# Performance work log

Measured on AMD Instinct MI355X. Metric: run time of the kernel, lower is better.

Reference implementation:

```python
import jax, jax.numpy as jnp
import numpy as np

EMBED_DIM = 2048
NUM_HEADS = 32
NUM_KV_HEADS = 8
HEAD_DIM = EMBED_DIM // NUM_HEADS          # 64
GROUP = NUM_HEADS // NUM_KV_HEADS          # 4 queries per KV head
BATCH, SEQ = 2, 2048


def setup_inputs() -> dict:
    key = jax.random.key(0)
    ks = jax.random.split(key, 9)
    s_in = 1.0 / np.sqrt(EMBED_DIM)
    kv_dim = NUM_KV_HEADS * HEAD_DIM
    return {
        "x":      jax.random.normal(ks[0], (BATCH, SEQ, EMBED_DIM), jnp.float32),
        "Wq":     jax.random.normal(ks[1], (EMBED_DIM, EMBED_DIM), jnp.float32) * s_in,
        "bq":     jnp.zeros((EMBED_DIM,), jnp.float32),
        "Wk":     jax.random.normal(ks[2], (EMBED_DIM, kv_dim), jnp.float32) * s_in,
        "bk":     jnp.zeros((kv_dim,), jnp.float32),
        "Wv":     jax.random.normal(ks[3], (EMBED_DIM, kv_dim), jnp.float32) * s_in,
        "bv":     jnp.zeros((kv_dim,), jnp.float32),
        "Wo":     jax.random.normal(ks[4], (EMBED_DIM, EMBED_DIM), jnp.float32) * s_in,
        "bo":     jnp.zeros((EMBED_DIM,), jnp.float32),
    }


def reference(x, Wq, bq, Wk, bk, Wv, bv, Wo, bo):
    B, S, _ = x.shape
    # Projections (torch Linear == x @ W + b with W stored as [in, out] here)
    q = (x @ Wq + bq).reshape(B, S, NUM_KV_HEADS, GROUP, HEAD_DIM)  # grouped heads
    k = (x @ Wk + bk).reshape(B, S, NUM_KV_HEADS, HEAD_DIM)
    v = (x @ Wv + bv).reshape(B, S, NUM_KV_HEADS, HEAD_DIM)

    scale = 1.0 / np.sqrt(HEAD_DIM)
    # scores[b, h, g, s, t] = q[b, s, h, g, :] . k[b, t, h, :]
    # (repeat_interleave of K across the group dim == broadcasting over g)
    scores = jnp.einsum("bshgd,bthd->bhgst", q, k) * scale
    attn = jax.nn.softmax(scores, axis=-1)
    out = jnp.einsum("bhgst,bthd->bshgd", attn, v)  # [B, S, kvh, g, D]
    out = out.reshape(B, S, EMBED_DIM)
    return out @ Wo + bo
```

## Files before the change

### kernel.cpp

```cpp
#include <hip/hip_runtime.h>


typedef __attribute__((ext_vector_type(8)))  short     s16x8;
typedef __attribute__((ext_vector_type(8)))  _Float16  h8;
typedef __attribute__((ext_vector_type(2)))  __fp16    fp16x2;
typedef __attribute__((ext_vector_type(4)))  float     f32x4;
typedef __attribute__((ext_vector_type(16))) float     f32x16;

#define DEVI static __device__ __forceinline__

#if __has_builtin(__builtin_amdgcn_exp2f)
#define EXP2F __builtin_amdgcn_exp2f
#else
#define EXP2F exp2f
#endif

DEVI short f2h(float f){ _Float16 h = (_Float16)f; return __builtin_bit_cast(short, h); }
DEVI unsigned pkh(float a, float b){
  fp16x2 t = __builtin_amdgcn_cvt_pkrtz(a, b);
  return __builtin_bit_cast(unsigned, t);
}

typedef __attribute__((address_space(3))) unsigned       lds_u32;
typedef __attribute__((address_space(1))) const unsigned gbl_u32;
DEVI void glds16(const short* g, short* l){
  __builtin_amdgcn_global_load_lds((gbl_u32*)g, (lds_u32*)l, 16, 0, 0);
}

__global__ void cast_kernel(const float* __restrict__ in, short* __restrict__ out, int n){
  int i = (blockIdx.x * 256 + threadIdx.x) * 8;
  if(i >= n) return;
  float4 a = *(const float4*)(in + i);
  float4 b = *(const float4*)(in + i + 4);
  s16x8 v;
  v[0]=f2h(a.x); v[1]=f2h(a.y); v[2]=f2h(a.z); v[3]=f2h(a.w);
  v[4]=f2h(b.x); v[5]=f2h(b.y); v[6]=f2h(b.z); v[7]=f2h(b.w);
  *(s16x8*)(out + i) = v;
}

__global__ void prep_kernel(const float* __restrict__ Wq, const float* __restrict__ Wk,
                            const float* __restrict__ Wv, const float* __restrict__ Wo,
                            const float* __restrict__ bq, const float* __restrict__ bk,
                            const float* __restrict__ bv,
                            short* __restrict__ WT, short* __restrict__ WoT,
                            float* __restrict__ bqkv){
  __shared__ __align__(16) short tile[64*72];
  const int gy = blockIdx.y;
  const int t = threadIdx.x;
  if(gy >= 80){
    int i = blockIdx.x * 256 + t;
    if(i < 3072) bqkv[i] = (i < 2048) ? bq[i] : (i < 2560 ? bk[i-2048] : bv[i-2560]);
    return;
  }
  const float* src; short* dst; int ldin, by;
  if(gy < 32)      { src = Wq; dst = WT;             ldin = 2048; by = gy;    }
  else if(gy < 40) { src = Wk; dst = WT + 2048*2048; ldin =  512; by = gy-32; }
  else if(gy < 48) { src = Wv; dst = WT + 2560*2048; ldin =  512; by = gy-40; }
  else             { src = Wo; dst = WoT;            ldin = 2048; by = gy-48; }
  const int tr = blockIdx.x * 64;
  const int tc = by * 64;
  for(int c = t; c < 512; c += 256){
    int r = c >> 3, g = c & 7;
    const float* p = src + (size_t)(tr + r) * ldin + tc + g*8;
    s16x8 v;
    #pragma unroll
    for(int e = 0; e < 8; e++) v[e] = f2h(p[e]);
    *(s16x8*)&tile[r*72 + g*8] = v;
  }
  __syncthreads();
  for(int c = t; c < 512; c += 256){
    int r = c >> 3, g = c & 7;
    s16x8 v;
    #pragma unroll
    for(int e = 0; e < 8; e++) v[e] = tile[(g*8+e)*72 + r];
    *(s16x8*)(dst + (size_t)(tc + r) * 2048 + tr + g*8) = v;
  }
}

template<bool OUT_F32>
__global__ __launch_bounds__(256, 2)
void gemm_bt_kernel(const short* __restrict__ A, const short* __restrict__ BT,
                    const float* __restrict__ bias, void* __restrict__ C,
                    int M, int N, int K, int scale_cols, float qscale){
  __shared__ __align__(16) short As[2][128*32];
  __shared__ __align__(16) short Bs[2][128*32];
  const int m0 = blockIdx.x * 128;
  const int n0 = blockIdx.y * 128;
  const int tid = threadIdx.x;
  const int wave = tid >> 6, lane = tid & 63;
  const int l16 = lane & 15, quad = lane >> 4;
  const int wm = (wave >> 1) * 64, wn = (wave & 1) * 64;

  const short* gA = A  + (size_t)(m0 + wave*32 + (lane>>2))*K + (lane&3)*8;
  const short* gB = BT + (size_t)(n0 + wave*32 + (lane>>2))*K + (lane&3)*8;
  short* lA0 = As[0] + wave*1024;
  short* lA1 = As[1] + wave*1024;
  short* lB0 = Bs[0] + wave*1024;
  short* lB1 = Bs[1] + wave*1024;

  f32x4 acc[4][4];
  #pragma unroll
  for(int i=0;i<4;i++)
    #pragma unroll
    for(int j=0;j<4;j++) acc[i][j] = (f32x4)(0.0f);

  for(int k0 = 0; k0 < K; k0 += 64){
    glds16(gA + k0,                     lA0);
    glds16(gA + 16*(size_t)K + k0,      lA0 + 512);
    glds16(gA + k0 + 32,                lA1);
    glds16(gA + 16*(size_t)K + k0 + 32, lA1 + 512);
    glds16(gB + k0,                     lB0);
    glds16(gB + 16*(size_t)K + k0,      lB0 + 512);
    glds16(gB + k0 + 32,                lB1);
    glds16(gB + 16*(size_t)K + k0 + 32, lB1 + 512);
    __syncthreads();
    h8 af[4], bfr[4];
    #pragma unroll
    for(int i=0;i<4;i++){
      af[i]  = *(const h8*)&As[0][(wm + i*16 + l16)*32 + quad*8];
      bfr[i] = *(const h8*)&Bs[0][(wn + i*16 + l16)*32 + quad*8];
    }
    #pragma unroll
    for(int i=0;i<4;i++)
      #pragma unroll
      for(int j=0;j<4;j++)
        acc[i][j] = __builtin_amdgcn_mfma_f32_16x16x32_f16(af[i], bfr[j], acc[i][j], 0, 0, 0);
    #pragma unroll
    for(int i=0;i<4;i++){
      af[i]  = *(const h8*)&As[1][(wm + i*16 + l16)*32 + quad*8];
      bfr[i] = *(const h8*)&Bs[1][(wn + i*16 + l16)*32 + quad*8];
    }
    #pragma unroll
    for(int i=0;i<4;i++)
      #pragma unroll
      for(int j=0;j<4;j++)
        acc[i][j] = __builtin_amdgcn_mfma_f32_16x16x32_f16(af[i], bfr[j], acc[i][j], 0, 0, 0);
    __syncthreads();
  }

  #pragma unroll
  for(int j=0;j<4;j++){
    int col = n0 + wn + j*16 + l16;
    float bb = bias[col];
    float sc = (col < scale_cols) ? qscale : 1.0f;
    #pragma unroll
    for(int i=0;i<4;i++){
      #pragma unroll
      for(int r=0;r<4;r++){
        size_t row = (size_t)(m0 + wm + i*16 + quad*4 + r);
        float v = (acc[i][j][r] + bb) * sc;
        if(OUT_F32) ((float*)C)[row*(size_t)N + col] = v;
        else        ((short*)C)[row*(size_t)N + col] = f2h(v);
      }
    }
  }
}

__global__ void fragpack_kernel(const short* __restrict__ QKV,
                                short* __restrict__ Kf, short* __restrict__ Vf){
  __shared__ __align__(16) short kt[64*72];
  __shared__ __align__(16) short vt[64*72];
  const int t = blockIdx.x, kvh = blockIdx.y, b = blockIdx.z;
  const int tid = threadIdx.x;
  const size_t rowbase = (size_t)(b*2048 + t*64);
  for(int c = tid; c < 512; c += 256){
    int r = c >> 3, g = c & 7;
    const short* src = QKV + (rowbase + r)*3072 + kvh*64 + g*8;
    *(s16x8*)&kt[r*72 + g*8] = *(const s16x8*)(src + 2048);
    *(s16x8*)&vt[r*72 + g*8] = *(const s16x8*)(src + 2560);
  }
  __syncthreads();
  const size_t obase = ((size_t)(b*8 + kvh)*32 + t) * 4096;
  for(int ch = tid; ch < 512; ch += 256){
    int kb = ch >> 8, l = ch & 63;
    int c = l & 31, h = l >> 5;
    int ks2 = (ch >> 6) & 3;
    *(s16x8*)(Kf + obase + (size_t)ch*8) =
        *(const s16x8*)&kt[(kb*32 + c)*72 + ks2*16 + h*8];
    int ksp = (ch >> 7) & 1, mb = (ch >> 6) & 1;
    int k0 = kb*32 + ksp*16 + h*4;
    int d  = mb*32 + c;
    s16x8 v;
    #pragma unroll
    for(int j = 0; j < 4; j++){
      v[j]   = vt[(k0 + j)*72 + d];
      v[4+j] = vt[(k0 + 8 + j)*72 + d];
    }
    *(s16x8*)(Vf + obase + (size_t)ch*8) = v;
  }
}

__global__ __launch_bounds__(256, 2)
void attn_kernel(const short* __restrict__ Qg, const short* __restrict__ Kf,
                 const short* __restrict__ Vf, short* __restrict__ Og, int ldq){
  const int L = blockIdx.x;
  const int nid = (L & 7)*64 + (L >> 3);
  const int qt  = nid & 31;
  const int grp = nid >> 5;
  const int kvh = grp & 7, b = grp >> 3;
  const int tid = threadIdx.x;
  const int wave = tid >> 6, lane = tid & 63;
  const int c = lane & 31, h = lane >> 5;
  const int head = kvh*4 + wave;
  const int q0 = qt * 64;

  h8 qreg[4][2];
  #pragma unroll
  for(int ks2=0; ks2<4; ks2++)
    #pragma unroll
    for(int qg=0; qg<2; qg++)
      qreg[ks2][qg] = *(const h8*)(Qg + (size_t)(b*2048 + q0 + qg*32 + c)*ldq
                                      + head*64 + ks2*16 + h*8);

  float lsum[2] = {0.0f, 0.0f};
  f32x16 oacc[2][2];
  #pragma unroll
  for(int qg=0; qg<2; qg++)
    #pragma unroll
    for(int mb=0; mb<2; mb++) oacc[qg][mb] = (f32x16)(0.0f);

  const short* kp = Kf + (size_t)grp * 131072 + lane*8;
  const short* vp = Vf + (size_t)grp * 131072 + lane*8;

  h8 kA[4], vA[4], kB[4], vB[4];

  auto loadf = [&](size_t it, h8* K, h8* V){
    const short* kq = kp + it*2048;
    const short* vq = vp + it*2048;
    #pragma unroll
    for(int i=0;i<4;i++){
      K[i] = *(const h8*)(kq + i*512);
      V[i] = *(const h8*)(vq + i*512);
    }
  };

  auto compute = [&](const h8* K, const h8* V){
    f32x16 st[2];
    st[0] = (f32x16)(0.0f); st[1] = (f32x16)(0.0f);
    #pragma unroll
    for(int ks2=0; ks2<4; ks2++){
      st[0] = __builtin_amdgcn_mfma_f32_32x32x16_f16(K[ks2], qreg[ks2][0], st[0], 0, 0, 0);
      st[1] = __builtin_amdgcn_mfma_f32_32x32x16_f16(K[ks2], qreg[ks2][1], st[1], 0, 0, 0);
    }
    union H8U { h8 v; unsigned u[4]; };
    H8U pk[2][2];
    #pragma unroll
    for(int qg=0; qg<2; qg++){
      float sacc = 0.0f;
      #pragma unroll
      for(int j=0; j<4; j++){
        float pa = EXP2F(st[qg][2*j]);
        float pb = EXP2F(st[qg][2*j+1]);
        sacc += pa + pb;
        pk[qg][0].u[j] = pkh(pa, pb);
      }
      #pragma unroll
      for(int j=0; j<4; j++){
        float pa = EXP2F(st[qg][8+2*j]);
        float pb = EXP2F(st[qg][8+2*j+1]);
        sacc += pa + pb;
        pk[qg][1].u[j] = pkh(pa, pb);
      }
      lsum[qg] += sacc;
    }
    #pragma unroll
    for(int ksp=0; ksp<2; ksp++){
      #pragma unroll
      for(int mb=0; mb<2; mb++){
        oacc[0][mb] = __builtin_amdgcn_mfma_f32_32x32x16_f16(V[ksp*2+mb], pk[0][ksp].v, oacc[0][mb], 0, 0, 0);
        oacc[1][mb] = __builtin_amdgcn_mfma_f32_32x32x16_f16(V[ksp*2+mb], pk[1][ksp].v, oacc[1][mb], 0, 0, 0);
      }
    }
  };

  loadf(0, kA, vA);
  #pragma unroll 1
  for(int it = 0; it < 64; it += 2){
    loadf((size_t)(it+1), kB, vB);
    compute(kA, vA);
    loadf((size_t)(it+2 < 64 ? it+2 : 0), kA, vA);
    compute(kB, vB);
  }

  #pragma unroll
  for(int qg=0; qg<2; qg++){
    lsum[qg] += __shfl_xor(lsum[qg], 32);
    float li = 1.0f / lsum[qg];
    size_t rowoff = (size_t)(b*2048 + q0 + qg*32 + c)*2048 + head*64;
    #pragma unroll
    for(int mb=0; mb<2; mb++){
      #pragma unroll
      for(int g2=0; g2<4; g2++){
        int d0 = mb*32 + 8*g2 + 4*h;
        uint2 wv;
        wv.x = pkh(oacc[qg][mb][4*g2+0]*li, oacc[qg][mb][4*g2+1]*li);
        wv.y = pkh(oacc[qg][mb][4*g2+2]*li, oacc[qg][mb][4*g2+3]*li);
        *(uint2*)&Og[rowoff + d0] = wv;
      }
    }
  }
}

extern "C" void kernel_launch(void* const* d_in, const int* in_sizes, int n_in,
                              void* d_out, int out_size, void* d_ws, size_t ws_size,
                              hipStream_t stream){
  const float* x  = (const float*)d_in[0];
  const float* Wq = (const float*)d_in[1];
  const float* bq = (const float*)d_in[2];
  const float* Wk = (const float*)d_in[3];
  const float* bk = (const float*)d_in[4];
  const float* Wv = (const float*)d_in[5];
  const float* bv = (const float*)d_in[6];
  const float* Wo = (const float*)d_in[7];
  const float* bo = (const float*)d_in[8];

  char* ws = (char*)d_ws;
  short* WT   = (short*)(ws);
  short* WoT  = (short*)(ws + 25165824);
  short* xb   = (short*)(ws + 33554432);
  short* QKV  = (short*)(ws + 50331648);
  float* bqkv = (float*)(ws + 79691776);
  short* AO   = xb;
  short* Kf   = (short*)(ws);
  short* Vf   = (short*)(ws + 4194304);

  cast_kernel<<<4096, 256, 0, stream>>>(x, xb, 8388608);
  prep_kernel<<<dim3(32,81), 256, 0, stream>>>(Wq, Wk, Wv, Wo, bq, bk, bv, WT, WoT, bqkv);

  gemm_bt_kernel<false><<<dim3(32,24), 256, 0, stream>>>(xb, WT, bqkv, QKV,
                                                         4096, 3072, 2048,
                                                         2048, 0.1803368801111244f);

  fragpack_kernel<<<dim3(32,8,2), 256, 0, stream>>>(QKV, Kf, Vf);

  attn_kernel<<<512, 256, 0, stream>>>(QKV, Kf, Vf, AO, 3072);

  gemm_bt_kernel<true><<<dim3(32,16), 256, 0, stream>>>(AO, WoT, bo, (float*)d_out,
                                                        4096, 2048, 2048, 0, 1.0f);
}
```

Measured before the change: 299.7 us.

## Double-buffer GEMM LDS tiles to prefetch next K-slice during MFMA compute

The projection GEMM now allocates two LDS stages per operand. It issues the global-to-LDS loads for the next 64-wide K slice before running the MFMAs on the current slice, and drops the barrier that sat between load and compute in each iteration. The goal is to hide global memory latency behind matrix math. In exchange, LDS use per block doubles to 64KB, which could limit how many blocks fit on a CU. Correctness also depends on the end-of-loop barrier waiting for the outstanding async LDS loads.

```diff
diff --git a/kernel.cpp b/kernel.cpp
--- a/kernel.cpp
+++ b/kernel.cpp
@@ -82,8 +82,8 @@
 void gemm_bt_kernel(const short* __restrict__ A, const short* __restrict__ BT,
                     const float* __restrict__ bias, void* __restrict__ C,
                     int M, int N, int K, int scale_cols, float qscale){
-  __shared__ __align__(16) short As[2][128*32];
-  __shared__ __align__(16) short Bs[2][128*32];
+  __shared__ __align__(16) short As[16384];
+  __shared__ __align__(16) short Bs[16384];
   const int m0 = blockIdx.x * 128;
   const int n0 = blockIdx.y * 128;
   const int tid = threadIdx.x;
@@ -93,10 +93,8 @@
 
   const short* gA = A  + (size_t)(m0 + wave*32 + (lane>>2))*K + (lane&3)*8;
   const short* gB = BT + (size_t)(n0 + wave*32 + (lane>>2))*K + (lane&3)*8;
-  short* lA0 = As[0] + wave*1024;
-  short* lA1 = As[1] + wave*1024;
-  short* lB0 = Bs[0] + wave*1024;
-  short* lB1 = Bs[1] + wave*1024;
+  short* lAw = As + wave*1024;
+  short* lBw = Bs + wave*1024;
 
   f32x4 acc[4][4];
   #pragma unroll
@@ -104,21 +102,30 @@
     #pragma unroll
     for(int j=0;j<4;j++) acc[i][j] = (f32x4)(0.0f);
 
+#define STAGE(BUF, K0) do{                                                    \
+    short* a_ = lAw + (BUF)*8192;                                             \
+    short* b_ = lBw + (BUF)*8192;                                             \
+    glds16(gA + (K0),                     a_);                                \
+    glds16(gA + 16*(size_t)K + (K0),      a_ + 512);                          \
+    glds16(gA + (K0) + 32,                a_ + 4096);                         \
+    glds16(gA + 16*(size_t)K + (K0) + 32, a_ + 4096 + 512);                   \
+    glds16(gB + (K0),                     b_);                                \
+    glds16(gB + 16*(size_t)K + (K0),      b_ + 512);                          \
+    glds16(gB + (K0) + 32,                b_ + 4096);                         \
+    glds16(gB + 16*(size_t)K + (K0) + 32, b_ + 4096 + 512);                   \
+  }while(0)
+
+  STAGE(0, 0);
+  __syncthreads();
+  int cur = 0;
   for(int k0 = 0; k0 < K; k0 += 64){
-    glds16(gA + k0,                     lA0);
-    glds16(gA + 16*(size_t)K + k0,      lA0 + 512);
-    glds16(gA + k0 + 32,                lA1);
-    glds16(gA + 16*(size_t)K + k0 + 32, lA1 + 512);
-    glds16(gB + k0,                     lB0);
-    glds16(gB + 16*(size_t)K + k0,      lB0 + 512);
-    glds16(gB + k0 + 32,                lB1);
-    glds16(gB + 16*(size_t)K + k0 + 32, lB1 + 512);
-    __syncthreads();
+    if(k0 + 64 < K) STAGE(cur^1, k0 + 64);
     h8 af[4], bfr[4];
+    const int bb = cur*8192;
     #pragma unroll
     for(int i=0;i<4;i++){
-      af[i]  = *(const h8*)&As[0][(wm + i*16 + l16)*32 + quad*8];
-      bfr[i] = *(const h8*)&Bs[0][(wn + i*16 + l16)*32 + quad*8];
+      af[i]  = *(const h8*)&As[bb + (wm + i*16 + l16)*32 + quad*8];
+      bfr[i] = *(const h8*)&Bs[bb + (wn + i*16 + l16)*32 + quad*8];
     }
     #pragma unroll
     for(int i=0;i<4;i++)
@@ -127,8 +134,8 @@
         acc[i][j] = __builtin_amdgcn_mfma_f32_16x16x32_f16(af[i], bfr[j], acc[i][j], 0, 0, 0);
     #pragma unroll
     for(int i=0;i<4;i++){
-      af[i]  = *(const h8*)&As[1][(wm + i*16 + l16)*32 + quad*8];
-      bfr[i] = *(const h8*)&Bs[1][(wn + i*16 + l16)*32 + quad*8];
+      af[i]  = *(const h8*)&As[bb + 4096 + (wm + i*16 + l16)*32 + quad*8];
+      bfr[i] = *(const h8*)&Bs[bb + 4096 + (wn + i*16 + l16)*32 + quad*8];
     }
     #pragma unroll
     for(int i=0;i<4;i++)
@@ -136,7 +143,9 @@
       for(int j=0;j<4;j++)
         acc[i][j] = __builtin_amdgcn_mfma_f32_16x16x32_f16(af[i], bfr[j], acc[i][j], 0, 0, 0);
     __syncthreads();
-  }
+    cur ^= 1;
+  }
+#undef STAGE
 
   #pragma unroll
   for(int j=0;j<4;j++){
```

Measured after the change: 311.5 us. 1.04x slower.
